# Optimization experiments

Hardware: AMD Instinct MI355X
Metric: run time of the kernel (lower is better)

Reference implementation:

```python
import jax, jax.numpy as jnp
import numpy as np

NUM_CLASSES = 1000
N, D = 65536, 512

def setup_inputs() -> dict:
    key = jax.random.key(0)
    k1, k2, k3 = jax.random.split(key, 3)
    x = jax.random.normal(k1, (N, D), dtype=jnp.float32)
    labels = jax.random.randint(k2, (N,), 0, NUM_CLASSES, dtype=jnp.int64)
    centers = jax.random.normal(k3, (NUM_CLASSES, D), dtype=jnp.float32)
    return {"x": x, "labels": labels, "centers": centers}

def reference(x, labels, centers):
    # diff of each sample to its own class center: [N, D]
    diff = x - centers[labels]
    # per-sample squared distance: [N]
    sq = jnp.sum(diff * diff, axis=-1)
    # segment-sum squared distances into classes, then Frobenius norm per class
    per_class_sq = jax.ops.segment_sum(sq, labels, num_segments=NUM_CLASSES)
    distance = jnp.sum(jnp.sqrt(per_class_sq))
    return distance / NUM_CLASSES
```

## Files before the change

kernel.cpp:

```cpp
#include <hip/hip_runtime.h>
#include <math.h>

#define NROWS 65536
#define DDIM 512
#define NUM_CLASSES 1000

#define SQ_OFF 0
#define PART_OFF NROWS
#define NBIN_BLOCKS 16
#define ROWS_PER_BIN_BLOCK (NROWS / NBIN_BLOCKS)
#define WS_NEED ((size_t)(NROWS + NBIN_BLOCKS * NUM_CLASSES) * 4)

__device__ inline float sqdiff4(float4 a, float4 b) {
    float dx = a.x - b.x, dy = a.y - b.y, dz = a.z - b.z, dw = a.w - b.w;
    return fmaf(dx, dx, fmaf(dy, dy, fmaf(dz, dz, dw * dw)));
}

__global__ __launch_bounds__(256) void CenterLoss_sq(
    const float* __restrict__ x,
    const int* __restrict__ labels,
    const float* __restrict__ centers,
    float* __restrict__ ws)
{
    const int wave = threadIdx.x >> 6;
    const int lane = threadIdx.x & 63;
    const int row  = (blockIdx.x << 2) + wave;
    const int lbl  = labels[row];

    const float4* __restrict__ xr =
        reinterpret_cast<const float4*>(x + (size_t)row * DDIM);
    const float4* __restrict__ cr =
        reinterpret_cast<const float4*>(centers + (size_t)lbl * DDIM);

    const float4 xv0 = xr[lane];
    const float4 xv1 = xr[lane + 64];
    const float4 cv0 = cr[lane];
    const float4 cv1 = cr[lane + 64];

    float acc = sqdiff4(xv0, cv0) + sqdiff4(xv1, cv1);

#pragma unroll
    for (int off = 32; off > 0; off >>= 1)
        acc += __shfl_xor(acc, off, 64);

    if (lane == 0)
        ws[SQ_OFF + row] = acc;
}

__global__ __launch_bounds__(1024) void CenterLoss_bin(
    const int* __restrict__ labels,
    float* __restrict__ ws)
{
    __shared__ float bins[NUM_CLASSES];
    const int t = threadIdx.x;
    if (t < NUM_CLASSES) bins[t] = 0.0f;
    __syncthreads();

    const int base = blockIdx.x * ROWS_PER_BIN_BLOCK;
#pragma unroll
    for (int i = 0; i < ROWS_PER_BIN_BLOCK / 1024; ++i) {
        const int r = base + i * 1024 + t;
        const float v = ws[SQ_OFF + r];
        const int   l = labels[r];
        atomicAdd(&bins[l], v);
    }

    __syncthreads();
    if (t < NUM_CLASSES)
        ws[PART_OFF + blockIdx.x * NUM_CLASSES + t] = bins[t];
}

__global__ __launch_bounds__(256) void CenterLoss_finalize(
    const float* __restrict__ ws, float* __restrict__ out)
{
    const int t = threadIdx.x;
    const int lane = t & 63;

    float s = 0.0f;
    if (t < NUM_CLASSES / 4) {
        float4 v = reinterpret_cast<const float4*>(ws + PART_OFF)[t];
#pragma unroll
        for (int b = 1; b < NBIN_BLOCKS; ++b) {
            float4 u = reinterpret_cast<const float4*>(
                           ws + PART_OFF + (size_t)b * NUM_CLASSES)[t];
            v.x += u.x; v.y += u.y; v.z += u.z; v.w += u.w;
        }
        s = sqrtf(v.x) + sqrtf(v.y) + sqrtf(v.z) + sqrtf(v.w);
    }
#pragma unroll
    for (int off = 32; off > 0; off >>= 1)
        s += __shfl_xor(s, off, 64);

    __shared__ float partial[4];
    if (lane == 0) partial[t >> 6] = s;
    __syncthreads();
    if (t == 0)
        out[0] = (partial[0] + partial[1] + partial[2] + partial[3])
                 / (float)NUM_CLASSES;
}

#define NSHARD 8
__global__ __launch_bounds__(256) void CL_zero8(float* __restrict__ ws) {
    const int n = NSHARD * 1024;
    for (int i = threadIdx.x + blockIdx.x * 256; i < n; i += 256 * 8) ws[i] = 0.0f;
}
__global__ __launch_bounds__(256) void CL_accum8(
    const float* __restrict__ x, const int* __restrict__ labels,
    const float* __restrict__ centers, float* __restrict__ ws)
{
    const int wave = threadIdx.x >> 6, lane = threadIdx.x & 63;
    const int row = (blockIdx.x << 2) + wave;
    const int lbl = labels[row];
    const float4* xr = (const float4*)(x + (size_t)row * DDIM);
    const float4* cr = (const float4*)(centers + (size_t)lbl * DDIM);
    const float4 xv0 = xr[lane], xv1 = xr[lane + 64];
    const float4 cv0 = cr[lane], cv1 = cr[lane + 64];
    float acc = sqdiff4(xv0, cv0) + sqdiff4(xv1, cv1);
#pragma unroll
    for (int off = 32; off > 0; off >>= 1) acc += __shfl_xor(acc, off, 64);
    if (lane == 0)
        atomicAdd(&ws[((blockIdx.x & (NSHARD - 1)) << 10) + lbl], acc);
}
__global__ __launch_bounds__(256) void CL_final8(
    const float* __restrict__ ws, float* __restrict__ out)
{
    const int t = threadIdx.x, lane = t & 63;
    float s = 0.0f;
    if (t < NUM_CLASSES / 4) {
        float4 v = reinterpret_cast<const float4*>(ws)[t];
#pragma unroll
        for (int sh = 1; sh < NSHARD; ++sh) {
            float4 u = reinterpret_cast<const float4*>(ws + (sh << 10))[t];
            v.x += u.x; v.y += u.y; v.z += u.z; v.w += u.w;
        }
        s = sqrtf(v.x) + sqrtf(v.y) + sqrtf(v.z) + sqrtf(v.w);
    }
#pragma unroll
    for (int off = 32; off > 0; off >>= 1) s += __shfl_xor(s, off, 64);
    __shared__ float partial[4];
    if (lane == 0) partial[t >> 6] = s;
    __syncthreads();
    if (t == 0)
        out[0] = (partial[0] + partial[1] + partial[2] + partial[3]) / (float)NUM_CLASSES;
}

extern "C" void kernel_launch(void* const* d_in, const int* in_sizes, int n_in,
                              void* d_out, int out_size, void* d_ws, size_t ws_size,
                              hipStream_t stream) {
    const float* x       = (const float*)d_in[0];
    const int*   labels  = (const int*)d_in[1];
    const float* centers = (const float*)d_in[2];
    float* out = (float*)d_out;
    float* ws  = (float*)d_ws;

    if (ws_size >= WS_NEED) {
        CenterLoss_sq<<<NROWS / 4, 256, 0, stream>>>(x, labels, centers, ws);
        CenterLoss_bin<<<NBIN_BLOCKS, 1024, 0, stream>>>(labels, ws);
        CenterLoss_finalize<<<1, 256, 0, stream>>>(ws, out);
    } else {
        CL_zero8<<<8, 256, 0, stream>>>(ws);
        CL_accum8<<<NROWS / 4, 256, 0, stream>>>(x, labels, centers, ws);
        CL_final8<<<1, 256, 0, stream>>>(ws, out);
    }
}
```

Measured before the change: 38.47 us.

## Counting-sort rows by label to reuse center rows across grouped samples

Result: slower. 41.14 us (+6.9%).

```diff
diff --git a/kernel.cpp b/kernel.cpp
--- a/kernel.cpp
+++ b/kernel.cpp
@@ -4,85 +4,150 @@
 #define NROWS 65536
 #define DDIM 512
 #define NUM_CLASSES 1000
-
-#define SQ_OFF 0
-#define PART_OFF NROWS
-#define NBIN_BLOCKS 16
-#define ROWS_PER_BIN_BLOCK (NROWS / NBIN_BLOCKS)
-#define WS_NEED ((size_t)(NROWS + NBIN_BLOCKS * NUM_CLASSES) * 4)
+#define NHB 16
+#define RPHB (NROWS / NHB)
+#define NSHARD 8
+
+#define HIST_OFF 0
+#define SORT_OFF 16384
+#define BINS_OFF (16384 + NROWS)
+#define WS_NEED ((size_t)(BINS_OFF + NSHARD * 1024) * 4)
 
 __device__ inline float sqdiff4(float4 a, float4 b) {
     float dx = a.x - b.x, dy = a.y - b.y, dz = a.z - b.z, dw = a.w - b.w;
     return fmaf(dx, dx, fmaf(dy, dy, fmaf(dz, dz, dw * dw)));
 }
 
-__global__ __launch_bounds__(256) void CenterLoss_sq(
+__global__ __launch_bounds__(1024) void CL_hist(
+    const int* __restrict__ labels, int* __restrict__ wsI)
+{
+    __shared__ int cnt[NUM_CLASSES];
+    const int t = threadIdx.x;
+    if (t < NUM_CLASSES) cnt[t] = 0;
+    __syncthreads();
+    const int base = blockIdx.x * RPHB;
+#pragma unroll
+    for (int i = 0; i < RPHB / 1024; ++i)
+        atomicAdd(&cnt[labels[base + i * 1024 + t]], 1);
+    __syncthreads();
+    if (t < NUM_CLASSES)
+        wsI[HIST_OFF + blockIdx.x * NUM_CLASSES + t] = cnt[t];
+}
+
+__global__ __launch_bounds__(1024) void CL_scatter(
+    const int* __restrict__ labels, int* __restrict__ wsI,
+    float* __restrict__ wsF)
+{
+    __shared__ int scanbuf[1024];
+    __shared__ int basech[NUM_CLASSES];
+    __shared__ int lcnt[NUM_CLASSES];
+    const int t = threadIdx.x;
+
+    if (blockIdx.x == 0) {
+#pragma unroll
+        for (int i = 0; i < NSHARD; ++i)
+            wsF[BINS_OFF + i * 1024 + t] = 0.0f;
+    }
+
+    int colsum = 0, myoff = 0;
+    if (t < NUM_CLASSES) {
+        for (int b = 0; b < NHB; ++b) {
+            const int v = wsI[HIST_OFF + b * NUM_CLASSES + t];
+            colsum += v;
+            if (b < (int)blockIdx.x) myoff += v;
+        }
+    }
+    scanbuf[t] = (t < NUM_CLASSES) ? colsum : 0;
+    __syncthreads();
+    for (int off = 1; off < 1024; off <<= 1) {
+        int v = scanbuf[t];
+        if (t >= off) v += scanbuf[t - off];
+        __syncthreads();
+        scanbuf[t] = v;
+        __syncthreads();
+    }
+    if (t < NUM_CLASSES) {
+        const int excl = (t == 0) ? 0 : scanbuf[t - 1];
+        basech[t] = excl + myoff;
+        lcnt[t] = 0;
+    }
+    __syncthreads();
+
+    const int base = blockIdx.x * RPHB;
+#pragma unroll
+    for (int i = 0; i < RPHB / 1024; ++i) {
+        const int r = base + i * 1024 + t;
+        const int l = labels[r];
+        const int pos = basech[l] + atomicAdd(&lcnt[l], 1);
+        wsI[SORT_OFF + pos] = r;
+    }
+}
+
+__global__ __launch_bounds__(256) void CL_accum_sorted(
     const float* __restrict__ x,
     const int* __restrict__ labels,
     const float* __restrict__ centers,
-    float* __restrict__ ws)
-{
-    const int wave = threadIdx.x >> 6;
+    const int* __restrict__ wsI,
+    float* __restrict__ wsF)
+{
     const int lane = threadIdx.x & 63;
-    const int row  = (blockIdx.x << 2) + wave;
-    const int lbl  = labels[row];
-
-    const float4* __restrict__ xr =
-        reinterpret_cast<const float4*>(x + (size_t)row * DDIM);
-    const float4* __restrict__ cr =
-        reinterpret_cast<const float4*>(centers + (size_t)lbl * DDIM);
-
-    const float4 xv0 = xr[lane];
-    const float4 xv1 = xr[lane + 64];
-    const float4 cv0 = cr[lane];
-    const float4 cv1 = cr[lane + 64];
-
-    float acc = sqdiff4(xv0, cv0) + sqdiff4(xv1, cv1);
-
-#pragma unroll
-    for (int off = 32; off > 0; off >>= 1)
-        acc += __shfl_xor(acc, off, 64);
-
-    if (lane == 0)
-        ws[SQ_OFF + row] = acc;
-}
-
-__global__ __launch_bounds__(1024) void CenterLoss_bin(
-    const int* __restrict__ labels,
-    float* __restrict__ ws)
-{
-    __shared__ float bins[NUM_CLASSES];
-    const int t = threadIdx.x;
-    if (t < NUM_CLASSES) bins[t] = 0.0f;
-    __syncthreads();
-
-    const int base = blockIdx.x * ROWS_PER_BIN_BLOCK;
-#pragma unroll
-    for (int i = 0; i < ROWS_PER_BIN_BLOCK / 1024; ++i) {
-        const int r = base + i * 1024 + t;
-        const float v = ws[SQ_OFF + r];
-        const int   l = labels[r];
-        atomicAdd(&bins[l], v);
-    }
-
-    __syncthreads();
-    if (t < NUM_CLASSES)
-        ws[PART_OFF + blockIdx.x * NUM_CLASSES + t] = bins[t];
-}
-
-__global__ __launch_bounds__(256) void CenterLoss_finalize(
-    const float* __restrict__ ws, float* __restrict__ out)
-{
-    const int t = threadIdx.x;
-    const int lane = t & 63;
-
+    const int wid  = (blockIdx.x << 2) + (threadIdx.x >> 6);
+    const int base = wid * 8;
+
+    int sr = 0, sl = 0;
+    if (lane < 8) {
+        sr = wsI[SORT_OFF + base + lane];
+        sl = labels[sr];
+    }
+
+    float* __restrict__ bins =
+        wsF + BINS_OFF + ((blockIdx.x & (NSHARD - 1)) << 10);
+
+    float racc = 0.0f;
+    int cur = -1;
+    float4 c0, c1;
+#pragma unroll
+    for (int k = 0; k < 8; ++k) {
+        const int r = __shfl(sr, k, 64);
+        const int l = __shfl(sl, k, 64);
+        if (l != cur) {
+            if (cur >= 0) {
+                float red = racc;
+#pragma unroll
+                for (int off = 32; off > 0; off >>= 1)
+                    red += __shfl_xor(red, off, 64);
+                if (lane == 0) atomicAdd(&bins[cur], red);
+            }
+            cur = l;
+            const float4* __restrict__ cr =
+                reinterpret_cast<const float4*>(centers + (size_t)l * DDIM);
+            c0 = cr[lane];
+            c1 = cr[lane + 64];
+            racc = 0.0f;
+        }
+        const float4* __restrict__ xr =
+            reinterpret_cast<const float4*>(x + (size_t)r * DDIM);
+        racc += sqdiff4(xr[lane], c0) + sqdiff4(xr[lane + 64], c1);
+    }
+    {
+        float red = racc;
+#pragma unroll
+        for (int off = 32; off > 0; off >>= 1)
+            red += __shfl_xor(red, off, 64);
+        if (lane == 0) atomicAdd(&bins[cur], red);
+    }
+}
+
+__global__ __launch_bounds__(256) void CL_final8(
+    const float* __restrict__ bins, float* __restrict__ out)
+{
+    const int t = threadIdx.x, lane = t & 63;
     float s = 0.0f;
     if (t < NUM_CLASSES / 4) {
-        float4 v = reinterpret_cast<const float4*>(ws + PART_OFF)[t];
-#pragma unroll
-        for (int b = 1; b < NBIN_BLOCKS; ++b) {
-            float4 u = reinterpret_cast<const float4*>(
-                           ws + PART_OFF + (size_t)b * NUM_CLASSES)[t];
+        float4 v = reinterpret_cast<const float4*>(bins)[t];
+#pragma unroll
+        for (int sh = 1; sh < NSHARD; ++sh) {
+            float4 u = reinterpret_cast<const float4*>(bins + (sh << 10))[t];
             v.x += u.x; v.y += u.y; v.z += u.z; v.w += u.w;
         }
         s = sqrtf(v.x) + sqrtf(v.y) + sqrtf(v.z) + sqrtf(v.w);
@@ -90,7 +155,6 @@
 #pragma unroll
     for (int off = 32; off > 0; off >>= 1)
         s += __shfl_xor(s, off, 64);
-
     __shared__ float partial[4];
     if (lane == 0) partial[t >> 6] = s;
     __syncthreads();
@@ -99,7 +163,6 @@
                  / (float)NUM_CLASSES;
 }
 
-#define NSHARD 8
 __global__ __launch_bounds__(256) void CL_zero8(float* __restrict__ ws) {
     const int n = NSHARD * 1024;
     for (int i = threadIdx.x + blockIdx.x * 256; i < n; i += 256 * 8) ws[i] = 0.0f;
@@ -121,28 +184,6 @@
     if (lane == 0)
         atomicAdd(&ws[((blockIdx.x & (NSHARD - 1)) << 10) + lbl], acc);
 }
-__global__ __launch_bounds__(256) void CL_final8(
-    const float* __restrict__ ws, float* __restrict__ out)
-{
-    const int t = threadIdx.x, lane = t & 63;
-    float s = 0.0f;
-    if (t < NUM_CLASSES / 4) {
-        float4 v = reinterpret_cast<const float4*>(ws)[t];
-#pragma unroll
-        for (int sh = 1; sh < NSHARD; ++sh) {
-            float4 u = reinterpret_cast<const float4*>(ws + (sh << 10))[t];
-            v.x += u.x; v.y += u.y; v.z += u.z; v.w += u.w;
-        }
-        s = sqrtf(v.x) + sqrtf(v.y) + sqrtf(v.z) + sqrtf(v.w);
-    }
-#pragma unroll
-    for (int off = 32; off > 0; off >>= 1) s += __shfl_xor(s, off, 64);
-    __shared__ float partial[4];
-    if (lane == 0) partial[t >> 6] = s;
-    __syncthreads();
-    if (t == 0)
-        out[0] = (partial[0] + partial[1] + partial[2] + partial[3]) / (float)NUM_CLASSES;
-}
 
 extern "C" void kernel_launch(void* const* d_in, const int* in_sizes, int n_in,
                               void* d_out, int out_size, void* d_ws, size_t ws_size,
@@ -151,15 +192,17 @@
     const int*   labels  = (const int*)d_in[1];
     const float* centers = (const float*)d_in[2];
     float* out = (float*)d_out;
-    float* ws  = (float*)d_ws;
+    float* wsF = (float*)d_ws;
+    int*   wsI = (int*)d_ws;
 
     if (ws_size >= WS_NEED) {
-        CenterLoss_sq<<<NROWS / 4, 256, 0, stream>>>(x, labels, centers, ws);
-        CenterLoss_bin<<<NBIN_BLOCKS, 1024, 0, stream>>>(labels, ws);
-        CenterLoss_finalize<<<1, 256, 0, stream>>>(ws, out);
+        CL_hist<<<NHB, 1024, 0, stream>>>(labels, wsI);
+        CL_scatter<<<NHB, 1024, 0, stream>>>(labels, wsI, wsF);
+        CL_accum_sorted<<<NROWS / 32, 256, 0, stream>>>(x, labels, centers, wsI, wsF);
+        CL_final8<<<1, 256, 0, stream>>>(wsF + BINS_OFF, out);
     } else {
-        CL_zero8<<<8, 256, 0, stream>>>(ws);
-        CL_accum8<<<NROWS / 4, 256, 0, stream>>>(x, labels, centers, ws);
-        CL_final8<<<1, 256, 0, stream>>>(ws, out);
-    }
-}
+        CL_zero8<<<8, 256, 0, stream>>>(wsF);
+        CL_accum8<<<NROWS / 4, 256, 0, stream>>>(x, labels, centers, wsF);
+        CL_final8<<<1, 256, 0, stream>>>(wsF, out);
+    }
+}
```

## Stage center column slices in LDS and fuse distance with per-block class binning

Applied to the files above, without the earlier changes.

Result: faster. 32.66 us (-15.1%).

```diff
diff --git a/kernel.cpp b/kernel.cpp
--- a/kernel.cpp
+++ b/kernel.cpp
@@ -4,93 +4,105 @@
 #define NROWS 65536
 #define DDIM 512
 #define NUM_CLASSES 1000
+#define CG 16
+#define RC 16
+#define RPB (NROWS / RC)
+#define CSTRIDE 36
 
-#define SQ_OFF 0
-#define PART_OFF NROWS
-#define NBIN_BLOCKS 16
-#define ROWS_PER_BIN_BLOCK (NROWS / NBIN_BLOCKS)
-#define WS_NEED ((size_t)(NROWS + NBIN_BLOCKS * NUM_CLASSES) * 4)
+#define PART_OFF 0
+#define SQRT_OFF (256 * NUM_CLASSES)
+#define WS_NEED ((size_t)(SQRT_OFF + NUM_CLASSES) * 4)
 
 __device__ inline float sqdiff4(float4 a, float4 b) {
     float dx = a.x - b.x, dy = a.y - b.y, dz = a.z - b.z, dw = a.w - b.w;
     return fmaf(dx, dx, fmaf(dy, dy, fmaf(dz, dz, dw * dw)));
 }
 
-__global__ __launch_bounds__(256) void CenterLoss_sq(
+__global__ __launch_bounds__(1024) void CL_slice(
     const float* __restrict__ x,
     const int* __restrict__ labels,
     const float* __restrict__ centers,
-    float* __restrict__ ws)
+    float* __restrict__ partials)
 {
-    const int wave = threadIdx.x >> 6;
-    const int lane = threadIdx.x & 63;
-    const int row  = (blockIdx.x << 2) + wave;
-    const int lbl  = labels[row];
+    __shared__ float cs[NUM_CLASSES * CSTRIDE];
+    __shared__ float bins[NUM_CLASSES];
+    const int t  = threadIdx.x;
+    const int cg = blockIdx.x & (CG - 1);
+    const int rc = blockIdx.x >> 4;
+    const int cq = t & 7;
+    const int tr = t >> 3;
 
-    const float4* __restrict__ xr =
-        reinterpret_cast<const float4*>(x + (size_t)row * DDIM);
-    const float4* __restrict__ cr =
-        reinterpret_cast<const float4*>(centers + (size_t)lbl * DDIM);
-
-    const float4 xv0 = xr[lane];
-    const float4 xv1 = xr[lane + 64];
-    const float4 cv0 = cr[lane];
-    const float4 cv1 = cr[lane + 64];
-
-    float acc = sqdiff4(xv0, cv0) + sqdiff4(xv1, cv1);
-
-#pragma unroll
-    for (int off = 32; off > 0; off >>= 1)
-        acc += __shfl_xor(acc, off, 64);
-
-    if (lane == 0)
-        ws[SQ_OFF + row] = acc;
-}
-
-__global__ __launch_bounds__(1024) void CenterLoss_bin(
-    const int* __restrict__ labels,
-    float* __restrict__ ws)
-{
-    __shared__ float bins[NUM_CLASSES];
-    const int t = threadIdx.x;
+    for (int k = tr; k < NUM_CLASSES; k += 128) {
+        const float4 c = *reinterpret_cast<const float4*>(
+            centers + (size_t)k * DDIM + cg * 32 + cq * 4);
+        *reinterpret_cast<float4*>(cs + k * CSTRIDE + cq * 4) = c;
+    }
     if (t < NUM_CLASSES) bins[t] = 0.0f;
     __syncthreads();
 
-    const int base = blockIdx.x * ROWS_PER_BIN_BLOCK;
-#pragma unroll
-    for (int i = 0; i < ROWS_PER_BIN_BLOCK / 1024; ++i) {
-        const int r = base + i * 1024 + t;
-        const float v = ws[SQ_OFF + r];
-        const int   l = labels[r];
-        atomicAdd(&bins[l], v);
+    const int rowbase = rc * RPB;
+    const float* __restrict__ xcg = x + cg * 32 + cq * 4;
+
+#pragma unroll 4
+    for (int i = 0; i < RPB; i += 256) {
+        const int rA = rowbase + i + tr;
+        const int rB = rA + 128;
+        const float4 xa = *reinterpret_cast<const float4*>(xcg + (size_t)rA * DDIM);
+        const float4 xb = *reinterpret_cast<const float4*>(xcg + (size_t)rB * DDIM);
+        const int la = labels[rA];
+        const int lb = labels[rB];
+        const float4 ca = *reinterpret_cast<const float4*>(cs + la * CSTRIDE + cq * 4);
+        const float4 cb = *reinterpret_cast<const float4*>(cs + lb * CSTRIDE + cq * 4);
+
+        float sa = sqdiff4(xa, ca);
+        float sb = sqdiff4(xb, cb);
+        sa += __shfl_xor(sa, 1, 64);  sb += __shfl_xor(sb, 1, 64);
+        sa += __shfl_xor(sa, 2, 64);  sb += __shfl_xor(sb, 2, 64);
+        sa += __shfl_xor(sa, 4, 64);  sb += __shfl_xor(sb, 4, 64);
+        if (cq == 0) {
+            atomicAdd(&bins[la], sa);
+            atomicAdd(&bins[lb], sb);
+        }
     }
 
     __syncthreads();
     if (t < NUM_CLASSES)
-        ws[PART_OFF + blockIdx.x * NUM_CLASSES + t] = bins[t];
+        partials[(size_t)blockIdx.x * NUM_CLASSES + t] = bins[t];
 }
 
-__global__ __launch_bounds__(256) void CenterLoss_finalize(
-    const float* __restrict__ ws, float* __restrict__ out)
+__global__ __launch_bounds__(256) void CL_reduce(
+    const float* __restrict__ partials, float* __restrict__ sqv)
 {
-    const int t = threadIdx.x;
-    const int lane = t & 63;
+    const int t = threadIdx.x, lane = t & 63, w = t >> 6;
+    __shared__ float acc[4][4];
+#pragma unroll
+    for (int j = 0; j < 4; ++j) {
+        const int k = blockIdx.x * 4 + j;
+        float v = partials[(size_t)t * NUM_CLASSES + k];
+#pragma unroll
+        for (int off = 32; off > 0; off >>= 1)
+            v += __shfl_xor(v, off, 64);
+        if (lane == 0) acc[w][j] = v;
+    }
+    __syncthreads();
+    if (t < 4) {
+        const float s = acc[0][t] + acc[1][t] + acc[2][t] + acc[3][t];
+        sqv[blockIdx.x * 4 + t] = sqrtf(s);
+    }
+}
 
+__global__ __launch_bounds__(256) void CL_sum(
+    const float* __restrict__ sqv, float* __restrict__ out)
+{
+    const int t = threadIdx.x, lane = t & 63;
     float s = 0.0f;
     if (t < NUM_CLASSES / 4) {
-        float4 v = reinterpret_cast<const float4*>(ws + PART_OFF)[t];
-#pragma unroll
-        for (int b = 1; b < NBIN_BLOCKS; ++b) {
-            float4 u = reinterpret_cast<const float4*>(
-                           ws + PART_OFF + (size_t)b * NUM_CLASSES)[t];
-            v.x += u.x; v.y += u.y; v.z += u.z; v.w += u.w;
-        }
-        s = sqrtf(v.x) + sqrtf(v.y) + sqrtf(v.z) + sqrtf(v.w);
+        const float4 v = reinterpret_cast<const float4*>(sqv)[t];
+        s = (v.x + v.y) + (v.z + v.w);
     }
 #pragma unroll
     for (int off = 32; off > 0; off >>= 1)
         s += __shfl_xor(s, off, 64);
-
     __shared__ float partial[4];
     if (lane == 0) partial[t >> 6] = s;
     __syncthreads();
@@ -113,9 +125,7 @@
     const int lbl = labels[row];
     const float4* xr = (const float4*)(x + (size_t)row * DDIM);
     const float4* cr = (const float4*)(centers + (size_t)lbl * DDIM);
-    const float4 xv0 = xr[lane], xv1 = xr[lane + 64];
-    const float4 cv0 = cr[lane], cv1 = cr[lane + 64];
-    float acc = sqdiff4(xv0, cv0) + sqdiff4(xv1, cv1);
+    float acc = sqdiff4(xr[lane], cr[lane]) + sqdiff4(xr[lane + 64], cr[lane + 64]);
 #pragma unroll
     for (int off = 32; off > 0; off >>= 1) acc += __shfl_xor(acc, off, 64);
     if (lane == 0)
@@ -154,9 +164,9 @@
     float* ws  = (float*)d_ws;
 
     if (ws_size >= WS_NEED) {
-        CenterLoss_sq<<<NROWS / 4, 256, 0, stream>>>(x, labels, centers, ws);
-        CenterLoss_bin<<<NBIN_BLOCKS, 1024, 0, stream>>>(labels, ws);
-        CenterLoss_finalize<<<1, 256, 0, stream>>>(ws, out);
+        CL_slice<<<CG * RC, 1024, 0, stream>>>(x, labels, centers, ws + PART_OFF);
+        CL_reduce<<<NUM_CLASSES / 4, 256, 0, stream>>>(ws + PART_OFF, ws + SQRT_OFF);
+        CL_sum<<<1, 256, 0, stream>>>(ws + SQRT_OFF, out);
     } else {
         CL_zero8<<<8, 256, 0, stream>>>(ws);
         CL_accum8<<<NROWS / 4, 256, 0, stream>>>(x, labels, centers, ws);
```
